# Performance work log

Measured on AMD Instinct MI355X. Metric: run time of the kernel, lower is better.

Reference implementation:

```python
import jax, jax.numpy as jnp
import numpy as np

N = 50000
E = 1600000
F_IN = 128
MP_UNITS = [32, 32, 32, 32, 16, 16, 16, 16, 8, 8, 8, 8]
MLP_UNITS = [16, 16]
DELTA = 2.0


def _lin(k, fi, fo):
    kw, kb = jax.random.split(k)
    s = 1.0 / np.sqrt(fi)
    W = jax.random.uniform(kw, (fi, fo), minval=-s, maxval=s, dtype=jnp.float32)
    b = jax.random.uniform(kb, (fo,), minval=-s, maxval=s, dtype=jnp.float32)
    return W, b


def setup_inputs() -> dict:
    key = jax.random.key(0)
    ks = jax.random.split(key, 64)
    inp = {}
    inp['x'] = jax.random.normal(ks[0], (N, F_IN), dtype=jnp.float32)
    inp['edge_index'] = jax.random.randint(ks[1], (2, E), 0, N, dtype=jnp.int32)
    inp['edge_weight'] = jax.random.uniform(ks[2], (E,), dtype=jnp.float32)
    inp['Wi'], inp['bi'] = _lin(ks[3], F_IN, F_IN)
    d = F_IN
    for i, u in enumerate(MP_UNITS):
        inp['Wc%d' % i], inp['bc%d' % i] = _lin(ks[4 + i], d, u)
        d = u
    for i, u in enumerate(MLP_UNITS):
        inp['Wm%d' % i], inp['bm%d' % i] = _lin(ks[20 + i], d, u)
        d = u
    inp['Wf'], inp['bf'] = _lin(ks[30], d, 1)
    return inp


def reference(x, edge_index, edge_weight, Wi, bi,
              Wc0, bc0, Wc1, bc1, Wc2, bc2, Wc3, bc3, Wc4, bc4, Wc5, bc5,
              Wc6, bc6, Wc7, bc7, Wc8, bc8, Wc9, bc9, Wc10, bc10, Wc11, bc11,
              Wm0, bm0, Wm1, bm1, Wf, bf):
    n = x.shape[0]
    src, dst = edge_index[0], edge_index[1]
    # delta_gcn_matrix: P = (1-delta) I + delta * D^{-1/2} A D^{-1/2}
    deg = jax.ops.segment_sum(edge_weight, dst, num_segments=n)
    dinv = jnp.where(deg > 0, jax.lax.rsqrt(jnp.maximum(deg, 1e-12)), 0.0)
    w = DELTA * dinv[src] * edge_weight * dinv[dst]  # [E]
    self_w = 1.0 - DELTA

    h = x @ Wi + bi

    def conv(h, W, b):
        hw = h @ W                                        # [N, out]
        msg = hw[src] * w[:, None]                        # gather + scale [E, out]
        agg = jax.ops.segment_sum(msg, dst, num_segments=n)  # scatter-add
        return agg + self_w * hw + b                      # fold in self-loops

    convs = [(Wc0, bc0), (Wc1, bc1), (Wc2, bc2), (Wc3, bc3), (Wc4, bc4), (Wc5, bc5),
             (Wc6, bc6), (Wc7, bc7), (Wc8, bc8), (Wc9, bc9), (Wc10, bc10), (Wc11, bc11)]
    for W, b in convs:
        h = jnp.tanh(conv(h, W, b))
    for W, b in [(Wm0, bm0), (Wm1, bm1)]:
        h = jax.nn.relu(h @ W + b)
    return jnp.tanh(h @ Wf + bf)  # [N, 1]
```

## Files before the change

kernel.cpp:

```cpp
#include <hip/hip_runtime.h>


constexpr int kN = 50000;
constexpr int kE = 1600000;
constexpr float kSelfW = -1.0f;
constexpr int kCAP = 72;
constexpr int PAD_N = 50176;
constexpr int kPROWS = PAD_N / 8;
constexpr int E4  = kE / 4;
constexpr int E4B = (E4 + 255) / 256;
constexpr int NBG = (kN + 255) / 256;

typedef int      v4i __attribute__((ext_vector_type(4)));
typedef float    v4f __attribute__((ext_vector_type(4)));
typedef _Float16 h8v __attribute__((ext_vector_type(8)));

__device__ __forceinline__ int rowmap(int r) {
  return (r & 7) * kPROWS + (r >> 3);
}
__device__ __forceinline__ unsigned packcw(int colMapped, float w) {
  _Float16 h = (_Float16)w;
  unsigned short u;
  __builtin_memcpy(&u, &h, 2);
  return (unsigned)(unsigned short)colMapped | ((unsigned)u << 16);
}
__device__ __forceinline__ float unpw(unsigned e) {
  unsigned short u = (unsigned short)(e >> 16);
  _Float16 h;
  __builtin_memcpy(&h, &u, 2);
  return (float)h;
}
__device__ __forceinline__ unsigned pack2h(float a, float b) {
  _Float16 ha = (_Float16)a, hb = (_Float16)b;
  unsigned short ua, ub;
  __builtin_memcpy(&ua, &ha, 2);
  __builtin_memcpy(&ub, &hb, 2);
  return (unsigned)ua | ((unsigned)ub << 16);
}
__device__ __forceinline__ float fast_tanh(float x) {
  float t = __expf(2.0f * x);
  float r = __builtin_amdgcn_rcpf(t + 1.0f);
  return 1.0f - 2.0f * r;
}

__global__ __launch_bounds__(256)
void prep(int* __restrict__ cnt, const float* __restrict__ Wi,
          const float* __restrict__ bi, const float* __restrict__ Wc0,
          float* __restrict__ Weff, float* __restrict__ beff) {
  if (blockIdx.x < 49) {
    int i = blockIdx.x * 1024 + threadIdx.x * 4;
    *reinterpret_cast<int4*>(cnt + i) = make_int4(0, 0, 0, 0);
  } else {
    int idx = (blockIdx.x - 49) * 256 + threadIdx.x;
    if (idx >= 129 * 32) return;
    int r = idx >> 5, j = idx & 31;
    float acc = 0.0f;
    if (r < 128) {
      for (int k = 0; k < 128; ++k) acc += Wi[r * 128 + k] * Wc0[k * 32 + j];
      Weff[r * 32 + j] = acc;
    } else {
      for (int k = 0; k < 128; ++k) acc += bi[k] * Wc0[k * 32 + j];
      beff[j] = acc;
    }
  }
}

__global__ __launch_bounds__(256)
void cnt_rank_kernel(const int* __restrict__ dst, int* __restrict__ cnt,
                     int* __restrict__ rank, int e4) {
  int i = blockIdx.x * blockDim.x + threadIdx.x;
  if (i >= e4) return;
  int4 d = reinterpret_cast<const int4*>(dst)[i];
  int4 r;
  r.x = atomicAdd(&cnt[rowmap(d.x)], 1);
  r.y = atomicAdd(&cnt[rowmap(d.y)], 1);
  r.z = atomicAdd(&cnt[rowmap(d.z)], 1);
  r.w = atomicAdd(&cnt[rowmap(d.w)], 1);
  reinterpret_cast<int4*>(rank)[i] = r;
}

__global__ __launch_bounds__(256)
void gemm0(const float* __restrict__ X, const float* __restrict__ Weff,
           const float* __restrict__ beff, _Float16* __restrict__ Y, int n) {
  __shared__ float smem[4128];
  for (int idx = threadIdx.x; idx < 128 * 32; idx += 256) {
    int j = idx >> 7, k = idx & 127;
    smem[j * 128 + k] = Weff[k * 32 + j];
  }
  if (threadIdx.x < 32) smem[4096 + threadIdx.x] = beff[threadIdx.x];
  __syncthreads();
  int row = blockIdx.x * 256 + threadIdx.x;
  if (row >= n) return;
  float acc[32];
#pragma unroll
  for (int j = 0; j < 32; ++j) acc[j] = smem[4096 + j];
  const float4* xr = reinterpret_cast<const float4*>(X + (size_t)row * 128);
  const float4* Ws4 = reinterpret_cast<const float4*>(smem);
  for (int k4 = 0; k4 < 32; ++k4) {
    float4 a = xr[k4];
#pragma unroll
    for (int j = 0; j < 32; ++j) {
      float4 wv = Ws4[j * 32 + k4];
      acc[j] += a.x * wv.x + a.y * wv.y + a.z * wv.z + a.w * wv.w;
    }
  }
  h8v* yr = reinterpret_cast<h8v*>(Y + (size_t)rowmap(row) * 32);
#pragma unroll
  for (int j8 = 0; j8 < 4; ++j8) {
    h8v v;
#pragma unroll
    for (int q = 0; q < 8; ++q) v[q] = (_Float16)acc[8 * j8 + q];
    yr[j8] = v;
  }
}

__global__ __launch_bounds__(256)
void build_part(const int* __restrict__ src, const int* __restrict__ dst,
                const float* __restrict__ ew, const int* __restrict__ rank,
                unsigned* __restrict__ ecw, int e4) {
  int p = blockIdx.x & 7;
  int i = (blockIdx.x >> 3) * 256 + threadIdx.x;
  if (i >= e4) return;
  v4i sv = __builtin_nontemporal_load(reinterpret_cast<const v4i*>(src) + i);
  v4i dv = __builtin_nontemporal_load(reinterpret_cast<const v4i*>(dst) + i);
  v4i rv = __builtin_nontemporal_load(reinterpret_cast<const v4i*>(rank) + i);
  v4f wv = __builtin_nontemporal_load(reinterpret_cast<const v4f*>(ew) + i);
#pragma unroll
  for (int c = 0; c < 4; ++c) {
    int d = dv[c];
    if ((d & 7) == p) {
      int r = rv[c];
      if (r < kCAP)
        ecw[(size_t)(p * kPROWS + (d >> 3)) * kCAP + r] =
            packcw(rowmap(sv[c]), wv[c]);
    }
  }
}

__global__ __launch_bounds__(256)
void deg_dinv_wave(const int* __restrict__ cnt, const unsigned* __restrict__ ecw,
                   float* __restrict__ dinv) {
  int lane = threadIdx.x & 63;
  int br = blockIdx.x * 4 + (threadIdx.x >> 6);
  int deg = min(cnt[br], kCAP);
  size_t base = (size_t)br * kCAP;
  float d = 0.0f;
  for (int i = lane; i < deg; i += 64) d += unpw(ecw[base + i]);
#pragma unroll
  for (int off = 32; off > 0; off >>= 1) d += __shfl_xor(d, off, 64);
  if (lane == 0) dinv[br] = (d > 0.0f) ? rsqrtf(fmaxf(d, 1e-12f)) : 0.0f;
}

__global__ __launch_bounds__(256)
void wscale_wave(const int* __restrict__ cnt, unsigned* __restrict__ ecw,
                 const float* __restrict__ dinv) {
  int lane = threadIdx.x & 63;
  int br = blockIdx.x * 4 + (threadIdx.x >> 6);
  int deg = min(cnt[br], kCAP);
  size_t base = (size_t)br * kCAP;
  float dr = 2.0f * dinv[br];
  for (int i = lane; i < kCAP; i += 64) {
    if (i < deg) {
      unsigned e = ecw[base + i];
      int cm = e & 0xFFFFu;
      ecw[base + i] = packcw(cm, dr * dinv[cm] * unpw(e));
    } else {
      ecw[base + i] = 0u;
    }
  }
}

template <int DOUT, int DNEXT, bool FINAL>
__global__ __launch_bounds__(256)
void spmm_fused(const _Float16* __restrict__ HW, const int* __restrict__ cnt,
                const unsigned* __restrict__ ecw, const float* __restrict__ b,
                const float* __restrict__ Wn, void* __restrict__ Out,
                const float* __restrict__ Wm0, const float* __restrict__ bm0,
                const float* __restrict__ Wm1, const float* __restrict__ bm1,
                const float* __restrict__ Wf, const float* __restrict__ bf,
                int n) {
  constexpr int R = 64 / DOUT;
  constexpr int W = DOUT;
  constexpr int L = DOUT / 8;
  constexpr int S = 8;
  constexpr int WST = DNEXT + 1;
  constexpr int JPT = (DNEXT > 0) ? (DNEXT / S) : 1;
  __shared__ float smem[(DNEXT > 0) ? DOUT * WST : 448];
  if constexpr (DNEXT > 0) {
    for (int idx = threadIdx.x; idx < DOUT * DNEXT; idx += 256) {
      int k = idx / DNEXT, j = idx - k * DNEXT;
      smem[k * WST + j] = Wn[idx];
    }
    __syncthreads();
  }
  if constexpr (FINAL) {
    int t = threadIdx.x;
    if (t < 128) smem[t] = Wm0[t];
    if (t < 256) smem[128 + t] = Wm1[t];
    if (t < 16) {
      smem[384 + t] = bm0[t];
      smem[400 + t] = bm1[t];
      smem[416 + t] = Wf[t];
    }
    if (t == 0) smem[432] = bf[0];
    __syncthreads();
  }
  int lane = threadIdx.x & 63;
  int wid = threadIdx.x >> 6;
  int g = lane / W;
  int gl = lane - g * W;
  int ch8 = gl & (L - 1);
  int sub = gl / L;
  int p = blockIdx.x & 7;
  int q = blockIdx.x >> 3;
  int brLocal = q * (4 * R) + wid * R + g;
  int br = p * kPROWS + brLocal;
  int deg = min(cnt[br], kCAP);
  const uint4* ecw4 = reinterpret_cast<const uint4*>(ecw + (size_t)br * kCAP);
  const h8v* HW8 = reinterpret_cast<const h8v*>(HW);
  uint4 ea = ecw4[sub];
  uint4 eb = ecw4[8 + sub];
  h8v a0 = HW8[(size_t)(ea.x & 0xFFFFu) * L + ch8];
  h8v a1 = HW8[(size_t)(ea.y & 0xFFFFu) * L + ch8];
  h8v a2 = HW8[(size_t)(ea.z & 0xFFFFu) * L + ch8];
  h8v a3 = HW8[(size_t)(ea.w & 0xFFFFu) * L + ch8];
  h8v b0 = HW8[(size_t)(eb.x & 0xFFFFu) * L + ch8];
  h8v b1 = HW8[(size_t)(eb.y & 0xFFFFu) * L + ch8];
  h8v b2 = HW8[(size_t)(eb.z & 0xFFFFu) * L + ch8];
  h8v b3 = HW8[(size_t)(eb.w & 0xFFFFu) * L + ch8];
  float wa0 = unpw(ea.x), wa1 = unpw(ea.y), wa2 = unpw(ea.z), wa3 = unpw(ea.w);
  float wb0 = unpw(eb.x), wb1 = unpw(eb.y), wb2 = unpw(eb.z), wb3 = unpw(eb.w);
  float acc[8];
#pragma unroll
  for (int q8 = 0; q8 < 8; ++q8)
    acc[q8] = wa0 * (float)a0[q8] + wa1 * (float)a1[q8] +
              wa2 * (float)a2[q8] + wa3 * (float)a3[q8] +
              wb0 * (float)b0[q8] + wb1 * (float)b1[q8] +
              wb2 * (float)b2[q8] + wb3 * (float)b3[q8];
  if (deg > 64) {
    if (sub < 2) {
      uint4 et = ecw4[16 + sub];
      h8v t0 = HW8[(size_t)(et.x & 0xFFFFu) * L + ch8];
      h8v t1 = HW8[(size_t)(et.y & 0xFFFFu) * L + ch8];
      h8v t2 = HW8[(size_t)(et.z & 0xFFFFu) * L + ch8];
      h8v t3 = HW8[(size_t)(et.w & 0xFFFFu) * L + ch8];
      float u0 = unpw(et.x), u1 = unpw(et.y), u2 = unpw(et.z), u3 = unpw(et.w);
#pragma unroll
      for (int q8 = 0; q8 < 8; ++q8)
        acc[q8] += u0 * (float)t0[q8] + u1 * (float)t1[q8] +
                   u2 * (float)t2[q8] + u3 * (float)t3[q8];
    }
  }
#pragma unroll
  for (int off = W / 2; off >= L; off >>= 1) {
#pragma unroll
    for (int q8 = 0; q8 < 8; ++q8) acc[q8] += __shfl_xor(acc[q8], off, 64);
  }
  int krow = 8 * ch8;
  h8v hsv = HW8[(size_t)br * L + ch8];
  float h[8];
#pragma unroll
  for (int q8 = 0; q8 < 8; ++q8)
    h[q8] = fast_tanh(acc[q8] + kSelfW * (float)hsv[q8] + b[krow + q8]);
  if constexpr (FINAL) {
    int row = (brLocal << 3) | p;
    if (gl == 0 && row < n) {
      float y0[16];
#pragma unroll
      for (int j = 0; j < 16; ++j) {
        float v = smem[384 + j];
#pragma unroll
        for (int k = 0; k < 8; ++k) v += h[k] * smem[k * 16 + j];
        y0[j] = fmaxf(v, 0.0f);
      }
      float y1[16];
#pragma unroll
      for (int j = 0; j < 16; ++j) {
        float v = smem[400 + j];
#pragma unroll
        for (int k = 0; k < 16; ++k) v += y0[k] * smem[128 + k * 16 + j];
        y1[j] = fmaxf(v, 0.0f);
      }
      float z = smem[432];
#pragma unroll
      for (int k = 0; k < 16; ++k) z += y1[k] * smem[416 + k];
      reinterpret_cast<float*>(Out)[row] = fast_tanh(z);
    }
  } else {
    float pj[JPT];
    int jbase = sub * JPT;
#pragma unroll
    for (int jj = 0; jj < JPT; ++jj) {
      int j = jbase + jj;
      float v = 0.0f;
#pragma unroll
      for (int q8 = 0; q8 < 8; ++q8) v += h[q8] * smem[(krow + q8) * WST + j];
      pj[jj] = v;
    }
#pragma unroll
    for (int off = 1; off < L; off <<= 1) {
#pragma unroll
      for (int jj = 0; jj < JPT; ++jj) pj[jj] += __shfl_xor(pj[jj], off, 64);
    }
    if (ch8 == 0) {
      _Float16* op = reinterpret_cast<_Float16*>(Out) + (size_t)br * DNEXT + jbase;
      if constexpr (JPT == 4) {
        uint2 u = make_uint2(pack2h(pj[0], pj[1]), pack2h(pj[2], pj[3]));
        *reinterpret_cast<uint2*>(op) = u;
      } else if constexpr (JPT == 2) {
        *reinterpret_cast<unsigned*>(op) = pack2h(pj[0], pj[1]);
      } else {
        op[0] = (_Float16)pj[0];
      }
    }
  }
}

extern "C" void kernel_launch(void* const* d_in, const int* in_sizes, int n_in,
                              void* d_out, int out_size, void* d_ws, size_t ws_size,
                              hipStream_t stream) {
  const float* x   = (const float*)d_in[0];
  const int*  eidx = (const int*)d_in[1];
  const float* ew  = (const float*)d_in[2];
  const float* Wi  = (const float*)d_in[3];
  const float* bi  = (const float*)d_in[4];
  const float* Wc[12]; const float* bc[12];
  for (int i = 0; i < 12; ++i) {
    Wc[i] = (const float*)d_in[5 + 2 * i];
    bc[i] = (const float*)d_in[6 + 2 * i];
  }
  const float* Wm0 = (const float*)d_in[29]; const float* bm0 = (const float*)d_in[30];
  const float* Wm1 = (const float*)d_in[31]; const float* bm1 = (const float*)d_in[32];
  const float* Wf  = (const float*)d_in[33]; const float* bf  = (const float*)d_in[34];
  float* out = (float*)d_out;

  const int* src = eidx;
  const int* dst = eidx + kE;

  float* wsf = (float*)d_ws;
  size_t off = 0;
  float*     dinv = wsf + off;              off += PAD_N;
  float*     Weff = wsf + off;              off += 128 * 32;
  float*     beff = wsf + off;              off += 64;
  int*       cnt  = (int*)(wsf + off);      off += PAD_N;
  unsigned*  ecw  = (unsigned*)(wsf + off); off += (size_t)PAD_N * kCAP;
  int*       rank = (int*)(wsf + off);      off += kE;
  _Float16*  B16  = (_Float16*)(wsf + off); off += (size_t)PAD_N * 16;
  _Float16*  C16  = (_Float16*)(wsf + off); off += (size_t)PAD_N * 16;

  const int dgb  = PAD_N / 4;
  const int sb32 = PAD_N / 8;
  const int sb16 = PAD_N / 16;
  const int sb8  = PAD_N / 32;

  prep<<<66, 256, 0, stream>>>(cnt, Wi, bi, Wc[0], Weff, beff);
  cnt_rank_kernel<<<E4B, 256, 0, stream>>>(dst, cnt, rank, E4);
  gemm0<<<NBG, 256, 0, stream>>>(x, Weff, beff, B16, kN);
  build_part<<<E4B * 8, 256, 0, stream>>>(src, dst, ew, rank, ecw, E4);
  deg_dinv_wave<<<dgb, 256, 0, stream>>>(cnt, ecw, dinv);
  wscale_wave<<<dgb, 256, 0, stream>>>(cnt, ecw, dinv);

  spmm_fused<32, 32, false><<<sb32, 256, 0, stream>>>(B16, cnt, ecw, bc[0], Wc[1], C16, nullptr, nullptr, nullptr, nullptr, nullptr, nullptr, kN);
  spmm_fused<32, 32, false><<<sb32, 256, 0, stream>>>(C16, cnt, ecw, bc[1], Wc[2], B16, nullptr, nullptr, nullptr, nullptr, nullptr, nullptr, kN);
  spmm_fused<32, 32, false><<<sb32, 256, 0, stream>>>(B16, cnt, ecw, bc[2], Wc[3], C16, nullptr, nullptr, nullptr, nullptr, nullptr, nullptr, kN);
  spmm_fused<32, 16, false><<<sb32, 256, 0, stream>>>(C16, cnt, ecw, bc[3], Wc[4], B16, nullptr, nullptr, nullptr, nullptr, nullptr, nullptr, kN);
  spmm_fused<16, 16, false><<<sb16, 256, 0, stream>>>(B16, cnt, ecw, bc[4], Wc[5], C16, nullptr, nullptr, nullptr, nullptr, nullptr, nullptr, kN);
  spmm_fused<16, 16, false><<<sb16, 256, 0, stream>>>(C16, cnt, ecw, bc[5], Wc[6], B16, nullptr, nullptr, nullptr, nullptr, nullptr, nullptr, kN);
  spmm_fused<16, 16, false><<<sb16, 256, 0, stream>>>(B16, cnt, ecw, bc[6], Wc[7], C16, nullptr, nullptr, nullptr, nullptr, nullptr, nullptr, kN);
  spmm_fused<16, 8, false><<<sb16, 256, 0, stream>>>(C16, cnt, ecw, bc[7], Wc[8], B16, nullptr, nullptr, nullptr, nullptr, nullptr, nullptr, kN);
  spmm_fused<8, 8, false><<<sb8, 256, 0, stream>>>(B16, cnt, ecw, bc[8], Wc[9], C16, nullptr, nullptr, nullptr, nullptr, nullptr, nullptr, kN);
  spmm_fused<8, 8, false><<<sb8, 256, 0, stream>>>(C16, cnt, ecw, bc[9], Wc[10], B16, nullptr, nullptr, nullptr, nullptr, nullptr, nullptr, kN);
  spmm_fused<8, 8, false><<<sb8, 256, 0, stream>>>(B16, cnt, ecw, bc[10], Wc[11], C16, nullptr, nullptr, nullptr, nullptr, nullptr, nullptr, kN);
  spmm_fused<8, 0, true><<<sb8, 256, 0, stream>>>(C16, cnt, ecw, bc[11], nullptr, out, Wm0, bm0, Wm1, bm1, Wf, bf, kN);
}
```

Before: 519.5 us.

## Fuse twelve SpMM layer launches into one persistent kernel with grid barriers

Replaces the twelve per-layer spmm_fused launches with a single persistent kernel of 1024 blocks. Each block loops over its rows and synchronises with the others through atomic grid barriers between layers. Every layer now writes to its own buffer, so no layer overwrites data another block may still be reading. This removes per-launch overhead and the inter-kernel drain gaps. In exchange it adds spin-barrier cost and relies on all 1024 blocks being co-resident, and the barrier has a timeout that could silently break correctness if they are not.

```diff
diff --git a/kernel.cpp b/kernel.cpp
--- a/kernel.cpp
+++ b/kernel.cpp
@@ -10,6 +10,7 @@
 constexpr int E4  = kE / 4;
 constexpr int E4B = (E4 + 255) / 256;
 constexpr int NBG = (kN + 255) / 256;
+constexpr int NBM = 1024;
 
 typedef int      v4i __attribute__((ext_vector_type(4)));
 typedef float    v4f __attribute__((ext_vector_type(4)));
@@ -43,15 +44,32 @@
   return 1.0f - 2.0f * r;
 }
 
+__device__ __forceinline__ void gsync(int* bars, int k) {
+  __syncthreads();
+  if (threadIdx.x == 0) {
+    __hip_atomic_fetch_add(&bars[k], 1, __ATOMIC_RELEASE,
+                           __HIP_MEMORY_SCOPE_AGENT);
+    int spins = 0;
+    while (__hip_atomic_load(&bars[k], __ATOMIC_RELAXED,
+                             __HIP_MEMORY_SCOPE_AGENT) < NBM) {
+      __builtin_amdgcn_s_sleep(2);
+      if (++spins > (1 << 18)) break;
+    }
+    (void)__hip_atomic_load(&bars[k], __ATOMIC_ACQUIRE,
+                            __HIP_MEMORY_SCOPE_WORKGROUP);
+  }
+  __syncthreads();
+}
+
 __global__ __launch_bounds__(256)
 void prep(int* __restrict__ cnt, const float* __restrict__ Wi,
           const float* __restrict__ bi, const float* __restrict__ Wc0,
           float* __restrict__ Weff, float* __restrict__ beff) {
-  if (blockIdx.x < 49) {
+  if (blockIdx.x < 50) {
     int i = blockIdx.x * 1024 + threadIdx.x * 4;
     *reinterpret_cast<int4*>(cnt + i) = make_int4(0, 0, 0, 0);
   } else {
-    int idx = (blockIdx.x - 49) * 256 + threadIdx.x;
+    int idx = (blockIdx.x - 50) * 256 + threadIdx.x;
     if (idx >= 129 * 32) return;
     int r = idx >> 5, j = idx & 31;
     float acc = 0.0f;
@@ -170,41 +188,41 @@
   }
 }
 
+struct MegaP {
+  const int* cnt; const unsigned* ecw; int* bars;
+  _Float16* buf[12];
+  const float* Wc[12]; const float* bc[12];
+  const float* Wm0; const float* bm0; const float* Wm1; const float* bm1;
+  const float* Wf; const float* bf; float* out;
+};
+
 template <int DOUT, int DNEXT, bool FINAL>
-__global__ __launch_bounds__(256)
-void spmm_fused(const _Float16* __restrict__ HW, const int* __restrict__ cnt,
-                const unsigned* __restrict__ ecw, const float* __restrict__ b,
-                const float* __restrict__ Wn, void* __restrict__ Out,
-                const float* __restrict__ Wm0, const float* __restrict__ bm0,
-                const float* __restrict__ Wm1, const float* __restrict__ bm1,
-                const float* __restrict__ Wf, const float* __restrict__ bf,
-                int n) {
+__device__ void spmm_phase(const MegaP& P, const _Float16* HW, void* Out,
+                           const float* Wn, const float* b, float* smem) {
   constexpr int R = 64 / DOUT;
   constexpr int W = DOUT;
   constexpr int L = DOUT / 8;
   constexpr int S = 8;
   constexpr int WST = DNEXT + 1;
   constexpr int JPT = (DNEXT > 0) ? (DNEXT / S) : 1;
-  __shared__ float smem[(DNEXT > 0) ? DOUT * WST : 448];
   if constexpr (DNEXT > 0) {
     for (int idx = threadIdx.x; idx < DOUT * DNEXT; idx += 256) {
       int k = idx / DNEXT, j = idx - k * DNEXT;
       smem[k * WST + j] = Wn[idx];
     }
-    __syncthreads();
   }
   if constexpr (FINAL) {
     int t = threadIdx.x;
-    if (t < 128) smem[t] = Wm0[t];
-    if (t < 256) smem[128 + t] = Wm1[t];
+    if (t < 128) smem[t] = P.Wm0[t];
+    if (t < 256) smem[128 + t] = P.Wm1[t];
     if (t < 16) {
-      smem[384 + t] = bm0[t];
-      smem[400 + t] = bm1[t];
-      smem[416 + t] = Wf[t];
-    }
-    if (t == 0) smem[432] = bf[0];
-    __syncthreads();
-  }
+      smem[384 + t] = P.bm0[t];
+      smem[400 + t] = P.bm1[t];
+      smem[416 + t] = P.Wf[t];
+    }
+    if (t == 0) smem[432] = P.bf[0];
+  }
+  __syncthreads();
   int lane = threadIdx.x & 63;
   int wid = threadIdx.x >> 6;
   int g = lane / W;
@@ -213,107 +231,126 @@
   int sub = gl / L;
   int p = blockIdx.x & 7;
   int q = blockIdx.x >> 3;
-  int brLocal = q * (4 * R) + wid * R + g;
-  int br = p * kPROWS + brLocal;
-  int deg = min(cnt[br], kCAP);
-  const uint4* ecw4 = reinterpret_cast<const uint4*>(ecw + (size_t)br * kCAP);
+  constexpr int PASS = 128 * 4 * R;
   const h8v* HW8 = reinterpret_cast<const h8v*>(HW);
-  uint4 ea = ecw4[sub];
-  uint4 eb = ecw4[8 + sub];
-  h8v a0 = HW8[(size_t)(ea.x & 0xFFFFu) * L + ch8];
-  h8v a1 = HW8[(size_t)(ea.y & 0xFFFFu) * L + ch8];
-  h8v a2 = HW8[(size_t)(ea.z & 0xFFFFu) * L + ch8];
-  h8v a3 = HW8[(size_t)(ea.w & 0xFFFFu) * L + ch8];
-  h8v b0 = HW8[(size_t)(eb.x & 0xFFFFu) * L + ch8];
-  h8v b1 = HW8[(size_t)(eb.y & 0xFFFFu) * L + ch8];
-  h8v b2 = HW8[(size_t)(eb.z & 0xFFFFu) * L + ch8];
-  h8v b3 = HW8[(size_t)(eb.w & 0xFFFFu) * L + ch8];
-  float wa0 = unpw(ea.x), wa1 = unpw(ea.y), wa2 = unpw(ea.z), wa3 = unpw(ea.w);
-  float wb0 = unpw(eb.x), wb1 = unpw(eb.y), wb2 = unpw(eb.z), wb3 = unpw(eb.w);
-  float acc[8];
-#pragma unroll
-  for (int q8 = 0; q8 < 8; ++q8)
-    acc[q8] = wa0 * (float)a0[q8] + wa1 * (float)a1[q8] +
-              wa2 * (float)a2[q8] + wa3 * (float)a3[q8] +
-              wb0 * (float)b0[q8] + wb1 * (float)b1[q8] +
-              wb2 * (float)b2[q8] + wb3 * (float)b3[q8];
-  if (deg > 64) {
-    if (sub < 2) {
-      uint4 et = ecw4[16 + sub];
-      h8v t0 = HW8[(size_t)(et.x & 0xFFFFu) * L + ch8];
-      h8v t1 = HW8[(size_t)(et.y & 0xFFFFu) * L + ch8];
-      h8v t2 = HW8[(size_t)(et.z & 0xFFFFu) * L + ch8];
-      h8v t3 = HW8[(size_t)(et.w & 0xFFFFu) * L + ch8];
-      float u0 = unpw(et.x), u1 = unpw(et.y), u2 = unpw(et.z), u3 = unpw(et.w);
-#pragma unroll
-      for (int q8 = 0; q8 < 8; ++q8)
-        acc[q8] += u0 * (float)t0[q8] + u1 * (float)t1[q8] +
-                   u2 * (float)t2[q8] + u3 * (float)t3[q8];
-    }
-  }
-#pragma unroll
-  for (int off = W / 2; off >= L; off >>= 1) {
-#pragma unroll
-    for (int q8 = 0; q8 < 8; ++q8) acc[q8] += __shfl_xor(acc[q8], off, 64);
-  }
-  int krow = 8 * ch8;
-  h8v hsv = HW8[(size_t)br * L + ch8];
-  float h[8];
-#pragma unroll
-  for (int q8 = 0; q8 < 8; ++q8)
-    h[q8] = fast_tanh(acc[q8] + kSelfW * (float)hsv[q8] + b[krow + q8]);
-  if constexpr (FINAL) {
-    int row = (brLocal << 3) | p;
-    if (gl == 0 && row < n) {
-      float y0[16];
-#pragma unroll
-      for (int j = 0; j < 16; ++j) {
-        float v = smem[384 + j];
-#pragma unroll
-        for (int k = 0; k < 8; ++k) v += h[k] * smem[k * 16 + j];
-        y0[j] = fmaxf(v, 0.0f);
+  for (int brL = (q * 4 + wid) * R + g; brL < kPROWS; brL += PASS) {
+    int br = p * kPROWS + brL;
+    int deg = min(P.cnt[br], kCAP);
+    const uint4* ecw4 = reinterpret_cast<const uint4*>(P.ecw + (size_t)br * kCAP);
+    uint4 ea = ecw4[sub];
+    uint4 eb = ecw4[8 + sub];
+    h8v a0 = HW8[(size_t)(ea.x & 0xFFFFu) * L + ch8];
+    h8v a1 = HW8[(size_t)(ea.y & 0xFFFFu) * L + ch8];
+    h8v a2 = HW8[(size_t)(ea.z & 0xFFFFu) * L + ch8];
+    h8v a3 = HW8[(size_t)(ea.w & 0xFFFFu) * L + ch8];
+    h8v b0 = HW8[(size_t)(eb.x & 0xFFFFu) * L + ch8];
+    h8v b1 = HW8[(size_t)(eb.y & 0xFFFFu) * L + ch8];
+    h8v b2 = HW8[(size_t)(eb.z & 0xFFFFu) * L + ch8];
+    h8v b3 = HW8[(size_t)(eb.w & 0xFFFFu) * L + ch8];
+    float wa0 = unpw(ea.x), wa1 = unpw(ea.y), wa2 = unpw(ea.z), wa3 = unpw(ea.w);
+    float wb0 = unpw(eb.x), wb1 = unpw(eb.y), wb2 = unpw(eb.z), wb3 = unpw(eb.w);
+    float acc[8];
+#pragma unroll
+    for (int q8 = 0; q8 < 8; ++q8)
+      acc[q8] = wa0 * (float)a0[q8] + wa1 * (float)a1[q8] +
+                wa2 * (float)a2[q8] + wa3 * (float)a3[q8] +
+                wb0 * (float)b0[q8] + wb1 * (float)b1[q8] +
+                wb2 * (float)b2[q8] + wb3 * (float)b3[q8];
+    if (deg > 64) {
+      if (sub < 2) {
+        uint4 et = ecw4[16 + sub];
+        h8v t0 = HW8[(size_t)(et.x & 0xFFFFu) * L + ch8];
+        h8v t1 = HW8[(size_t)(et.y & 0xFFFFu) * L + ch8];
+        h8v t2 = HW8[(size_t)(et.z & 0xFFFFu) * L + ch8];
+        h8v t3 = HW8[(size_t)(et.w & 0xFFFFu) * L + ch8];
+        float u0 = unpw(et.x), u1 = unpw(et.y), u2 = unpw(et.z), u3 = unpw(et.w);
+#pragma unroll
+        for (int q8 = 0; q8 < 8; ++q8)
+          acc[q8] += u0 * (float)t0[q8] + u1 * (float)t1[q8] +
+                     u2 * (float)t2[q8] + u3 * (float)t3[q8];
       }
-      float y1[16];
-#pragma unroll
-      for (int j = 0; j < 16; ++j) {
-        float v = smem[400 + j];
-#pragma unroll
-        for (int k = 0; k < 16; ++k) v += y0[k] * smem[128 + k * 16 + j];
-        y1[j] = fmaxf(v, 0.0f);
+    }
+#pragma unroll
+    for (int off = W / 2; off >= L; off >>= 1) {
+#pragma unroll
+      for (int q8 = 0; q8 < 8; ++q8) acc[q8] += __shfl_xor(acc[q8], off, 64);
+    }
+    int krow = 8 * ch8;
+    h8v hsv = HW8[(size_t)br * L + ch8];
+    float h[8];
+#pragma unroll
+    for (int q8 = 0; q8 < 8; ++q8)
+      h[q8] = fast_tanh(acc[q8] + kSelfW * (float)hsv[q8] + b[krow + q8]);
+    if constexpr (FINAL) {
+      int row = (brL << 3) | p;
+      if (gl == 0 && row < kN) {
+        float y0[16];
+#pragma unroll
+        for (int j = 0; j < 16; ++j) {
+          float v = smem[384 + j];
+#pragma unroll
+          for (int k = 0; k < 8; ++k) v += h[k] * smem[k * 16 + j];
+          y0[j] = fmaxf(v, 0.0f);
+        }
+        float y1[16];
+#pragma unroll
+        for (int j = 0; j < 16; ++j) {
+          float v = smem[400 + j];
+#pragma unroll
+          for (int k = 0; k < 16; ++k) v += y0[k] * smem[128 + k * 16 + j];
+          y1[j] = fmaxf(v, 0.0f);
+        }
+        float z = smem[432];
+#pragma unroll
+        for (int k = 0; k < 16; ++k) z += y1[k] * smem[416 + k];
+        reinterpret_cast<float*>(Out)[row] = fast_tanh(z);
       }
-      float z = smem[432];
-#pragma unroll
-      for (int k = 0; k < 16; ++k) z += y1[k] * smem[416 + k];
-      reinterpret_cast<float*>(Out)[row] = fast_tanh(z);
-    }
-  } else {
-    float pj[JPT];
-    int jbase = sub * JPT;
-#pragma unroll
-    for (int jj = 0; jj < JPT; ++jj) {
-      int j = jbase + jj;
-      float v = 0.0f;
-#pragma unroll
-      for (int q8 = 0; q8 < 8; ++q8) v += h[q8] * smem[(krow + q8) * WST + j];
-      pj[jj] = v;
-    }
-#pragma unroll
-    for (int off = 1; off < L; off <<= 1) {
-#pragma unroll
-      for (int jj = 0; jj < JPT; ++jj) pj[jj] += __shfl_xor(pj[jj], off, 64);
-    }
-    if (ch8 == 0) {
-      _Float16* op = reinterpret_cast<_Float16*>(Out) + (size_t)br * DNEXT + jbase;
-      if constexpr (JPT == 4) {
-        uint2 u = make_uint2(pack2h(pj[0], pj[1]), pack2h(pj[2], pj[3]));
-        *reinterpret_cast<uint2*>(op) = u;
-      } else if constexpr (JPT == 2) {
-        *reinterpret_cast<unsigned*>(op) = pack2h(pj[0], pj[1]);
-      } else {
-        op[0] = (_Float16)pj[0];
+    } else {
+      float pj[JPT];
+      int jbase = sub * JPT;
+#pragma unroll
+      for (int jj = 0; jj < JPT; ++jj) {
+        int j = jbase + jj;
+        float v = 0.0f;
+#pragma unroll
+        for (int q8 = 0; q8 < 8; ++q8) v += h[q8] * smem[(krow + q8) * WST + j];
+        pj[jj] = v;
       }
-    }
-  }
+#pragma unroll
+      for (int off = 1; off < L; off <<= 1) {
+#pragma unroll
+        for (int jj = 0; jj < JPT; ++jj) pj[jj] += __shfl_xor(pj[jj], off, 64);
+      }
+      if (ch8 == 0) {
+        _Float16* op = reinterpret_cast<_Float16*>(Out) + (size_t)br * DNEXT + jbase;
+        if constexpr (JPT == 4) {
+          uint2 u = make_uint2(pack2h(pj[0], pj[1]), pack2h(pj[2], pj[3]));
+          *reinterpret_cast<uint2*>(op) = u;
+        } else if constexpr (JPT == 2) {
+          *reinterpret_cast<unsigned*>(op) = pack2h(pj[0], pj[1]);
+        } else {
+          op[0] = (_Float16)pj[0];
+        }
+      }
+    }
+  }
+}
+
+__global__ __launch_bounds__(256, 4)
+void mega(MegaP P) {
+  __shared__ float smem[1100];
+  spmm_phase<32, 32, false>(P, P.buf[0], P.buf[1], P.Wc[1], P.bc[0], smem);  gsync(P.bars, 0);
+  spmm_phase<32, 32, false>(P, P.buf[1], P.buf[2], P.Wc[2], P.bc[1], smem);  gsync(P.bars, 1);
+  spmm_phase<32, 32, false>(P, P.buf[2], P.buf[3], P.Wc[3], P.bc[2], smem);  gsync(P.bars, 2);
+  spmm_phase<32, 16, false>(P, P.buf[3], P.buf[4], P.Wc[4], P.bc[3], smem);  gsync(P.bars, 3);
+  spmm_phase<16, 16, false>(P, P.buf[4], P.buf[5], P.Wc[5], P.bc[4], smem);  gsync(P.bars, 4);
+  spmm_phase<16, 16, false>(P, P.buf[5], P.buf[6], P.Wc[6], P.bc[5], smem);  gsync(P.bars, 5);
+  spmm_phase<16, 16, false>(P, P.buf[6], P.buf[7], P.Wc[7], P.bc[6], smem);  gsync(P.bars, 6);
+  spmm_phase<16, 8, false>(P, P.buf[7], P.buf[8], P.Wc[8], P.bc[7], smem);   gsync(P.bars, 7);
+  spmm_phase<8, 8, false>(P, P.buf[8], P.buf[9], P.Wc[9], P.bc[8], smem);    gsync(P.bars, 8);
+  spmm_phase<8, 8, false>(P, P.buf[9], P.buf[10], P.Wc[10], P.bc[9], smem);  gsync(P.bars, 9);
+  spmm_phase<8, 8, false>(P, P.buf[10], P.buf[11], P.Wc[11], P.bc[10], smem); gsync(P.bars, 10);
+  spmm_phase<8, 0, true>(P, P.buf[11], P.out, nullptr, P.bc[11], smem);
 }
 
 extern "C" void kernel_launch(void* const* d_in, const int* in_sizes, int n_in,
@@ -324,15 +361,15 @@
   const float* ew  = (const float*)d_in[2];
   const float* Wi  = (const float*)d_in[3];
   const float* bi  = (const float*)d_in[4];
-  const float* Wc[12]; const float* bc[12];
+  MegaP P;
   for (int i = 0; i < 12; ++i) {
-    Wc[i] = (const float*)d_in[5 + 2 * i];
-    bc[i] = (const float*)d_in[6 + 2 * i];
-  }
-  const float* Wm0 = (const float*)d_in[29]; const float* bm0 = (const float*)d_in[30];
-  const float* Wm1 = (const float*)d_in[31]; const float* bm1 = (const float*)d_in[32];
-  const float* Wf  = (const float*)d_in[33]; const float* bf  = (const float*)d_in[34];
-  float* out = (float*)d_out;
+    P.Wc[i] = (const float*)d_in[5 + 2 * i];
+    P.bc[i] = (const float*)d_in[6 + 2 * i];
+  }
+  P.Wm0 = (const float*)d_in[29]; P.bm0 = (const float*)d_in[30];
+  P.Wm1 = (const float*)d_in[31]; P.bm1 = (const float*)d_in[32];
+  P.Wf  = (const float*)d_in[33]; P.bf  = (const float*)d_in[34];
+  P.out = (float*)d_out;
 
   const int* src = eidx;
   const int* dst = eidx + kE;
@@ -343,33 +380,25 @@
   float*     Weff = wsf + off;              off += 128 * 32;
   float*     beff = wsf + off;              off += 64;
   int*       cnt  = (int*)(wsf + off);      off += PAD_N;
+  int*       bars = cnt + PAD_N;            off += 1024;
   unsigned*  ecw  = (unsigned*)(wsf + off); off += (size_t)PAD_N * kCAP;
   int*       rank = (int*)(wsf + off);      off += kE;
-  _Float16*  B16  = (_Float16*)(wsf + off); off += (size_t)PAD_N * 16;
-  _Float16*  C16  = (_Float16*)(wsf + off); off += (size_t)PAD_N * 16;
-
-  const int dgb  = PAD_N / 4;
-  const int sb32 = PAD_N / 8;
-  const int sb16 = PAD_N / 16;
-  const int sb8  = PAD_N / 32;
-
-  prep<<<66, 256, 0, stream>>>(cnt, Wi, bi, Wc[0], Weff, beff);
+  {
+    const int wdt[12] = {32, 32, 32, 32, 16, 16, 16, 16, 8, 8, 8, 8};
+    for (int l = 0; l < 12; ++l) {
+      P.buf[l] = (_Float16*)(wsf + off);
+      off += (size_t)PAD_N * wdt[l] / 2;
+    }
+  }
+  P.cnt = cnt; P.ecw = ecw; P.bars = bars;
+
+  const int dgb = PAD_N / 4;
+
+  prep<<<67, 256, 0, stream>>>(cnt, Wi, bi, P.Wc[0], Weff, beff);
   cnt_rank_kernel<<<E4B, 256, 0, stream>>>(dst, cnt, rank, E4);
-  gemm0<<<NBG, 256, 0, stream>>>(x, Weff, beff, B16, kN);
+  gemm0<<<NBG, 256, 0, stream>>>(x, Weff, beff, P.buf[0], kN);
   build_part<<<E4B * 8, 256, 0, stream>>>(src, dst, ew, rank, ecw, E4);
   deg_dinv_wave<<<dgb, 256, 0, stream>>>(cnt, ecw, dinv);
   wscale_wave<<<dgb, 256, 0, stream>>>(cnt, ecw, dinv);
-
-  spmm_fused<32, 32, false><<<sb32, 256, 0, stream>>>(B16, cnt, ecw, bc[0], Wc[1], C16, nullptr, nullptr, nullptr, nullptr, nullptr, nullptr, kN);
-  spmm_fused<32, 32, false><<<sb32, 256, 0, stream>>>(C16, cnt, ecw, bc[1], Wc[2], B16, nullptr, nullptr, nullptr, nullptr, nullptr, nullptr, kN);
-  spmm_fused<32, 32, false><<<sb32, 256, 0, stream>>>(B16, cnt, ecw, bc[2], Wc[3], C16, nullptr, nullptr, nullptr, nullptr, nullptr, nullptr, kN);
-  spmm_fused<32, 16, false><<<sb32, 256, 0, stream>>>(C16, cnt, ecw, bc[3], Wc[4], B16, nullptr, nullptr, nullptr, nullptr, nullptr, nullptr, kN);
-  spmm_fused<16, 16, false><<<sb16, 256, 0, stream>>>(B16, cnt, ecw, bc[4], Wc[5], C16, nullptr, nullptr, nullptr, nullptr, nullptr, nullptr, kN);
-  spmm_fused<16, 16, false><<<sb16, 256, 0, stream>>>(C16, cnt, ecw, bc[5], Wc[6], B16, nullptr, nullptr, nullptr, nullptr, nullptr, nullptr, kN);
-  spmm_fused<16, 16, false><<<sb16, 256, 0, stream>>>(B16, cnt, ecw, bc[6], Wc[7], C16, nullptr, nullptr, nullptr, nullptr, nullptr, nullptr, kN);
-  spmm_fused<16, 8, false><<<sb16, 256, 0, stream>>>(C16, cnt, ecw, bc[7], Wc[8], B16, nullptr, nullptr, nullptr, nullptr, nullptr, nullptr, kN);
-  spmm_fused<8, 8, false><<<sb8, 256, 0, stream>>>(B16, cnt, ecw, bc[8], Wc[9], C16, nullptr, nullptr, nullptr, nullptr, nullptr, nullptr, kN);
-  spmm_fused<8, 8, false><<<sb8, 256, 0, stream>>>(C16, cnt, ecw, bc[9], Wc[10], B16, nullptr, nullptr, nullptr, nullptr, nullptr, nullptr, kN);
-  spmm_fused<8, 8, false><<<sb8, 256, 0, stream>>>(B16, cnt, ecw, bc[10], Wc[11], C16, nullptr, nullptr, nullptr, nullptr, nullptr, nullptr, kN);
-  spmm_fused<8, 0, true><<<sb8, 256, 0, stream>>>(C16, cnt, ecw, bc[11], nullptr, out, Wm0, bm0, Wm1, bm1, Wf, bf, kN);
-}
+  mega<<<NBM, 256, 0, stream>>>(P);
+}
```

New measurement: 1.851 ms. 3.56x slower.
